# Performance work log

Measured on AMD Instinct MI355X. Metric: run time of the kernel, lower is better.

The kernel has to match this reference:

```python
import jax, jax.numpy as jnp
import numpy as np

VOCAB = 50000
EMB = 200        # embedding_size
CAP = 3          # capitalization_size
IN = EMB + CAP   # LSTM input size = 203
HID = 128        # LSTMCell(128)
B = 256
T = 500          # comment_length
NC = 6           # num_classes
DENSE = 64


def _lstm_scan(x_tbi, W, b):
    """x_tbi: [T,B,IN]. W: [IN+HID, 4*HID] (tf gate order i, j, f, o), b: [4*HID].
    Returns h sequence [T,B,HID]. forget_bias=1.0 as in tf.contrib.rnn.LSTMCell."""
    h0 = jnp.zeros((x_tbi.shape[1], HID), x_tbi.dtype)

    def step(carry, x):
        h, c = carry
        gates = jnp.concatenate([x, h], axis=-1) @ W + b   # [B, 4*HID]
        i, j, f, o = jnp.split(gates, 4, axis=-1)
        c = jax.nn.sigmoid(f + 1.0) * c + jax.nn.sigmoid(i) * jnp.tanh(j)
        h = jax.nn.sigmoid(o) * jnp.tanh(c)
        return (h, c), h

    _, hs = jax.lax.scan(step, (h0, h0), x_tbi)
    return hs


def setup_inputs() -> dict:
    key = jax.random.key(0)
    ks = jax.random.split(key, 12)
    words = jax.random.randint(ks[0], (B, T), 0, VOCAB, dtype=jnp.int32)
    capitals = jax.random.randint(ks[1], (B, T), 0, CAP, dtype=jnp.int32)
    # word embeddings: random trainable table with a trailing zero-padding row
    word_emb = jax.random.normal(ks[2], (VOCAB + 1, EMB), dtype=jnp.float32) * 0.1
    # capitalization embedding: one_hot_embedding_matrix(3) = [eye(3); zeros(1,3)]
    cap_emb = jnp.concatenate([jnp.eye(CAP, dtype=jnp.float32),
                               jnp.zeros((1, CAP), dtype=jnp.float32)], axis=0)
    def glorot(k, shape):
        lim = np.sqrt(6.0 / (shape[0] + shape[1]))
        return jax.random.uniform(k, shape, jnp.float32, -lim, lim)
    W_fw = glorot(ks[3], (IN + HID, 4 * HID))
    b_fw = jnp.zeros((4 * HID,), jnp.float32)
    W_bw = glorot(ks[4], (IN + HID, 4 * HID))
    b_bw = jnp.zeros((4 * HID,), jnp.float32)
    W1 = glorot(ks[5], (2 * HID, DENSE))
    b1 = jnp.zeros((DENSE,), jnp.float32)
    W2 = glorot(ks[6], (DENSE, NC))
    b2 = jnp.zeros((NC,), jnp.float32)
    return {"words": words, "capitals": capitals, "word_emb": word_emb,
            "cap_emb": cap_emb, "W_fw": W_fw, "b_fw": b_fw,
            "W_bw": W_bw, "b_bw": b_bw, "W1": W1, "b1": b1,
            "W2": W2, "b2": b2}


def reference(words, capitals, word_emb, cap_emb, W_fw, b_fw, W_bw, b_bw,
              W1, b1, W2, b2):
    # embedding lookups and concat -> [B, T, 203]
    x = jnp.concatenate([word_emb[words], cap_emb[capitals]], axis=-1)
    x_tbi = jnp.transpose(x, (1, 0, 2))                    # [T, B, IN]
    # forward direction: take output at last timestep
    h_fw_last = _lstm_scan(x_tbi, W_fw, b_fw)[-1]          # [B, HID]
    # backward direction: bidirectional_dynamic_rnn reverses bw outputs back,
    # so outputs[1][:, 0, :] == last state of scan over the reversed sequence
    h_bw_first = _lstm_scan(x_tbi[::-1], W_bw, b_bw)[-1]   # [B, HID]
    rnn_output = jnp.concatenate([h_fw_last, h_bw_first], axis=1)  # [B, 256]
    dense1 = jax.nn.elu(rnn_output @ W1 + b1)              # [B, 64]
    y_hat = jax.nn.sigmoid(dense1 @ W2 + b2)               # [B, NC]
    return y_hat
```

## Files before the change

kernel.cpp:

```cpp
#include <hip/hip_runtime.h>

#define T 500
#define NB 256
#define VROWS 50001
#define EMB 200
#define KPAD 224
#define MPAD 50048
#define LOG2E 1.44269504f

typedef unsigned short u16;
typedef __attribute__((ext_vector_type(8))) __bf16 bf16x8;
typedef __attribute__((ext_vector_type(8))) short short8;
typedef __attribute__((ext_vector_type(4))) float f32x4;
typedef __attribute__((ext_vector_type(4))) u16 u16x4;
typedef __attribute__((ext_vector_type(4))) int i32x4;

__device__ __forceinline__ u16 f2bf(float x) {
  __bf16 h = (__bf16)x;
  return __builtin_bit_cast(u16, h);
}
__device__ __forceinline__ float bf2f(u16 b) {
  union { unsigned u; float f; } v; v.u = ((unsigned)b) << 16;
  return v.f;
}
__device__ __forceinline__ float rcp_(float x) { return __builtin_amdgcn_rcpf(x); }
__device__ __forceinline__ float ex2_(float x) { return __builtin_amdgcn_exp2f(x); }
__device__ __forceinline__ float gsc(int g) { return (g == 1) ? 2.f * LOG2E : -LOG2E; }

__global__ void prep_kernel(const int* __restrict__ words, const int* __restrict__ caps,
                            const float* __restrict__ word_emb,
                            const float* __restrict__ cap_emb,
                            const float* __restrict__ Wfw, const float* __restrict__ bfw,
                            const float* __restrict__ Wbw, const float* __restrict__ bbw,
                            int* __restrict__ wordsT, int* __restrict__ capsT,
                            float* __restrict__ Cproj, u16* __restrict__ Apad,
                            u16* __restrict__ Bt) {
  const int S0 = NB * T;
  const int S1 = MPAD * (KPAD / 4);
  const int S2 = 2 * 512 * KPAD;
  const int S3 = 2 * 4 * 512;
  int tid = blockIdx.x * blockDim.x + threadIdx.x;
  int nthr = gridDim.x * blockDim.x;
  for (int i = tid; i < S0 + S1 + S2 + S3; i += nthr) {
    if (i < S0) {
      int b = i / T, t = i - b * T;
      wordsT[t * NB + b] = words[i];
      capsT[t * NB + b]  = caps[i];
    } else if (i < S0 + S1) {
      int idx = i - S0;
      int v = idx / (KPAD / 4), q = idx - v * (KPAD / 4);
      int k = q * 4;
      u16x4 o;
      if (v < VROWS && k < EMB) {
        const float* p = word_emb + (size_t)v * EMB + k;
        o[0] = f2bf(p[0]); o[1] = f2bf(p[1]); o[2] = f2bf(p[2]); o[3] = f2bf(p[3]);
      } else {
        o[0] = o[1] = o[2] = o[3] = 0;
      }
      *(u16x4*)(Apad + (size_t)v * KPAD + k) = o;
    } else if (i < S0 + S1 + S2) {
      int idx = i - S0 - S1;
      int d = idx / (512 * KPAD), rem = idx - d * (512 * KPAD);
      int colp = rem / KPAD, k = rem - colp * KPAD;
      const float* W = d ? Wbw : Wfw;
      int g = colp & 3, jj = colp >> 2;
      Bt[idx] = (k < EMB) ? f2bf(W[k * 512 + g * 128 + jj] * gsc(g)) : (u16)0;
    } else {
      int idx = i - S0 - S1 - S2;
      int dir = idx >> 11; int c = (idx >> 9) & 3; int colp = idx & 511;
      int j = colp >> 2, g = colp & 3;
      const float* W = dir ? Wbw : Wfw;
      const float* bias = dir ? bbw : bfw;
      float v = bias[g * 128 + j] + (g == 2 ? 1.f : 0.f);
      #pragma unroll
      for (int cc = 0; cc < 3; ++cc)
        v += cap_emb[c * 3 + cc] * W[(200 + cc) * 512 + g * 128 + j];
      Cproj[idx] = v * gsc(g);
    }
  }
}

__global__ __launch_bounds__(256) void vproj_kernel(
    const u16* __restrict__ Apad, const u16* __restrict__ Bt,
    u16* __restrict__ Vfw, u16* __restrict__ Vbw) {
  const int mt = blockIdx.x, nt = blockIdx.y, dir = blockIdx.z;
  const u16* __restrict__ B = Bt + (size_t)dir * 512 * KPAD;
  u16* __restrict__ V = dir ? Vbw : Vfw;

  __shared__ u16 Al[2][128 * 32];
  __shared__ u16 Bl[2][128 * 32];

  const int tid = threadIdx.x;
  const int w = tid >> 6, l = tid & 63;
  const int la = l & 15, lb = l >> 4;
  const int m0 = mt * 128, n0 = nt * 128;

  auto stage = [&](int buf, int ks) {
    int k0 = ks * 32;
    #pragma unroll
    for (int h = 0; h < 2; ++h) {
      int c = w * 128 + h * 64 + l;
      int row = c >> 2, kq = c & 3;
      const u16* ga = Apad + (size_t)(m0 + row) * KPAD + k0 + kq * 8;
      __builtin_amdgcn_global_load_lds(
          (const __attribute__((address_space(1))) void*)ga,
          (__attribute__((address_space(3))) void*)&Al[buf][(w * 128 + h * 64) * 8],
          16, 0, 0);
      const u16* gb = B + (size_t)(n0 + row) * KPAD + k0 + kq * 8;
      __builtin_amdgcn_global_load_lds(
          (const __attribute__((address_space(1))) void*)gb,
          (__attribute__((address_space(3))) void*)&Bl[buf][(w * 128 + h * 64) * 8],
          16, 0, 0);
    }
  };

  f32x4 z = {0.f, 0.f, 0.f, 0.f};
  f32x4 acc[4][4] = {{z,z,z,z},{z,z,z,z},{z,z,z,z},{z,z,z,z}};
  const int wr = w >> 1, wc = w & 1;

  stage(0, 0);
  __syncthreads();
  #pragma unroll 1
  for (int ks = 0; ks < 7; ++ks) {
    int cur = ks & 1;
    if (ks < 6) stage(cur ^ 1, ks + 1);
    bf16x8 af[4], bfr[4];
    #pragma unroll
    for (int m = 0; m < 4; ++m)
      af[m] = *(const bf16x8*)&Al[cur][(wr * 64 + m * 16 + la) * 32 + lb * 8];
    #pragma unroll
    for (int n = 0; n < 4; ++n)
      bfr[n] = *(const bf16x8*)&Bl[cur][(wc * 64 + n * 16 + la) * 32 + lb * 8];
    #pragma unroll
    for (int m = 0; m < 4; ++m)
      #pragma unroll
      for (int n = 0; n < 4; ++n)
        acc[m][n] = __builtin_amdgcn_mfma_f32_16x16x32_bf16(af[m], bfr[n], acc[m][n], 0, 0, 0);
    __syncthreads();
  }

  #pragma unroll
  for (int m = 0; m < 4; ++m) {
    #pragma unroll
    for (int n = 0; n < 4; ++n) {
      #pragma unroll
      for (int r = 0; r < 4; ++r) {
        int v = m0 + wr * 64 + m * 16 + lb * 4 + r;
        int colp = n0 + wc * 64 + n * 16 + la;
        V[(size_t)v * 512 + colp] = f2bf(acc[m][n][r]);
      }
    }
  }
}

template <int PAR>
__device__ __forceinline__ void lstm_step(
    int t, int dir, int b0, int la, int lb, int j,
    const int* __restrict__ wordsT, const int* __restrict__ capsT,
    const u16* __restrict__ V, const float* __restrict__ Cp,
    const bf16x8 (&bfrag)[4][4], u16* __restrict__ hbuf,
    u16x4 (&vw_c)[4], f32x4 (&cp_c)[4],
    i32x4& wi_c, i32x4& ci_c,
    i32x4& wi_g, i32x4& ci_g,
    u16x4 (&vw_g)[4], f32x4 (&cp_g)[4],
    f32x4& cst, f32x4& hl) {
  {
    int ts = t + 4; if (ts > T - 1) ts = T - 1;
    int tt = dir ? (T - 1 - ts) : ts;
    wi_c = *(const i32x4*)(wordsT + tt * NB + b0 + lb * 4);
    ci_c = *(const i32x4*)(capsT + tt * NB + b0 + lb * 4);
  }
  #pragma unroll
  for (int r = 0; r < 4; ++r) {
    vw_g[r] = *(const u16x4*)(V + (size_t)wi_g[r] * 512 + j * 4);
    cp_g[r] = *(const f32x4*)(Cp + ci_g[r] * 512 + j * 4);
  }

  const u16* hb = hbuf + PAR * 2048;
  const int swz = (la & 7) << 3;
  bf16x8 afr[4];
  #pragma unroll
  for (int kk = 0; kk < 4; ++kk)
    afr[kk] = *(const bf16x8*)(hb + ((la * 128 + kk * 32 + lb * 8) ^ swz));

  f32x4 acc0, acc1, acc2, acc3;
  #pragma unroll
  for (int r = 0; r < 4; ++r) {
    acc0[r] = bf2f(vw_c[r][0]) + cp_c[r][0];
    acc1[r] = bf2f(vw_c[r][1]) + cp_c[r][1];
    acc2[r] = bf2f(vw_c[r][2]) + cp_c[r][2];
    acc3[r] = bf2f(vw_c[r][3]) + cp_c[r][3];
  }
  #pragma unroll
  for (int kk = 0; kk < 4; ++kk) {
    acc0 = __builtin_amdgcn_mfma_f32_16x16x32_bf16(afr[kk], bfrag[0][kk], acc0, 0, 0, 0);
    acc1 = __builtin_amdgcn_mfma_f32_16x16x32_bf16(afr[kk], bfrag[1][kk], acc1, 0, 0, 0);
    acc2 = __builtin_amdgcn_mfma_f32_16x16x32_bf16(afr[kk], bfrag[2][kk], acc2, 0, 0, 0);
    acc3 = __builtin_amdgcn_mfma_f32_16x16x32_bf16(afr[kk], bfrag[3][kk], acc3, 0, 0, 0);
  }
  u16* ho = hbuf + (PAR ^ 1) * 2048;
  #pragma unroll
  for (int r = 0; r < 4; ++r) {
    float ig = rcp_(1.f + ex2_(acc0[r]));
    float tj = 1.f - 2.f * rcp_(1.f + ex2_(acc1[r]));
    float fg = rcp_(1.f + ex2_(acc2[r]));
    float cn = fg * cst[r] + ig * tj;
    cst[r] = cn;
    float og = rcp_(1.f + ex2_(acc3[r]));
    float hn = og * (1.f - 2.f * rcp_(1.f + ex2_(2.f * LOG2E * cn)));
    hl[r] = hn;
    int row = lb * 4 + r;
    ho[(row * 128 + j) ^ ((row & 7) << 3)] = f2bf(hn);
  }
  __builtin_amdgcn_sched_barrier(0);
  asm volatile("s_waitcnt lgkmcnt(0)");
  __builtin_amdgcn_s_barrier();
  __builtin_amdgcn_sched_barrier(0);
}

__global__ __launch_bounds__(512, 1) void lstm_kernel(
    const int* __restrict__ wordsT, const int* __restrict__ capsT,
    const u16* __restrict__ Vfw, const u16* __restrict__ Vbw,
    const float* __restrict__ CprojAll, const float* __restrict__ Wfw,
    const float* __restrict__ Wbw, float* __restrict__ rnn) {
  const int dir = blockIdx.x & 1;
  const int chunk = blockIdx.x >> 1;
  const int b0 = chunk * 16;
  const u16* __restrict__ V = dir ? Vbw : Vfw;
  const float* __restrict__ Cp = CprojAll + dir * 4 * 512;
  const float* __restrict__ W = dir ? Wbw : Wfw;

  const int tid = threadIdx.x;
  const int w = tid >> 6, l = tid & 63, la = l & 15, lb = l >> 4;
  const int j = w * 16 + la;

  bf16x8 bfrag[4][4];
  #pragma unroll
  for (int g = 0; g < 4; ++g) {
    #pragma unroll
    for (int kk = 0; kk < 4; ++kk) {
      short8 t8;
      #pragma unroll
      for (int r = 0; r < 8; ++r) {
        int k = kk * 32 + lb * 8 + r;
        t8[r] = (short)f2bf(W[(203 + k) * 512 + g * 128 + j] * gsc(g));
      }
      bfrag[g][kk] = __builtin_bit_cast(bf16x8, t8);
    }
  }

  __shared__ u16 hbuf[2 * 16 * 128];
  for (int i = tid; i < 2 * 16 * 128; i += 512) hbuf[i] = 0;

  f32x4 cst = {0.f, 0.f, 0.f, 0.f};
  f32x4 hl  = {0.f, 0.f, 0.f, 0.f};

  i32x4 wiA, ciA, wiB, ciB, wiC, ciC, wiD, ciD;
  u16x4 vwA[4], vwB[4], vwC[4], vwD[4];
  f32x4 cpA[4], cpB[4], cpC[4], cpD[4];
  {
    int t0 = dir ? (T - 1) : 0;
    int t1 = dir ? (T - 2) : 1;
    int t2 = dir ? (T - 3) : 2;
    int t3 = dir ? (T - 4) : 3;
    wiA = *(const i32x4*)(wordsT + t0 * NB + b0 + lb * 4);
    ciA = *(const i32x4*)(capsT + t0 * NB + b0 + lb * 4);
    wiB = *(const i32x4*)(wordsT + t1 * NB + b0 + lb * 4);
    ciB = *(const i32x4*)(capsT + t1 * NB + b0 + lb * 4);
    wiC = *(const i32x4*)(wordsT + t2 * NB + b0 + lb * 4);
    ciC = *(const i32x4*)(capsT + t2 * NB + b0 + lb * 4);
    wiD = *(const i32x4*)(wordsT + t3 * NB + b0 + lb * 4);
    ciD = *(const i32x4*)(capsT + t3 * NB + b0 + lb * 4);
  }
  #pragma unroll
  for (int r = 0; r < 4; ++r) {
    vwA[r] = *(const u16x4*)(V + (size_t)wiA[r] * 512 + j * 4);
    cpA[r] = *(const f32x4*)(Cp + ciA[r] * 512 + j * 4);
    vwB[r] = *(const u16x4*)(V + (size_t)wiB[r] * 512 + j * 4);
    cpB[r] = *(const f32x4*)(Cp + ciB[r] * 512 + j * 4);
  }
  __syncthreads();

  #pragma unroll 1
  for (int tq = 0; tq < T / 4; ++tq) {
    int t0 = 4 * tq;
    lstm_step<0>(t0,     dir, b0, la, lb, j, wordsT, capsT, V, Cp, bfrag, hbuf,
                 vwA, cpA, wiA, ciA, wiC, ciC, vwC, cpC, cst, hl);
    lstm_step<1>(t0 + 1, dir, b0, la, lb, j, wordsT, capsT, V, Cp, bfrag, hbuf,
                 vwB, cpB, wiB, ciB, wiD, ciD, vwD, cpD, cst, hl);
    lstm_step<0>(t0 + 2, dir, b0, la, lb, j, wordsT, capsT, V, Cp, bfrag, hbuf,
                 vwC, cpC, wiC, ciC, wiA, ciA, vwA, cpA, cst, hl);
    lstm_step<1>(t0 + 3, dir, b0, la, lb, j, wordsT, capsT, V, Cp, bfrag, hbuf,
                 vwD, cpD, wiD, ciD, wiB, ciB, vwB, cpB, cst, hl);
  }

  #pragma unroll
  for (int r = 0; r < 4; ++r)
    rnn[(size_t)(b0 + lb * 4 + r) * 256 + dir * 128 + j] = hl[r];
}

__global__ void head_kernel(const float* __restrict__ rnn, const float* __restrict__ W1,
                            const float* __restrict__ b1, const float* __restrict__ W2,
                            const float* __restrict__ b2, float* __restrict__ out) {
  int b = blockIdx.x;
  int jj = threadIdx.x;
  __shared__ float d1[64];
  float acc = b1[jj];
  const float* r = rnn + b * 256;
  #pragma unroll 4
  for (int k = 0; k < 256; ++k) acc += r[k] * W1[k * 64 + jj];
  d1[jj] = acc > 0.f ? acc : (__expf(acc) - 1.f);
  __syncthreads();
  if (jj < 6) {
    float a2 = b2[jj];
    #pragma unroll 8
    for (int k = 0; k < 64; ++k) a2 += d1[k] * W2[k * 6 + jj];
    out[b * 6 + jj] = rcp_(1.f + __expf(-a2));
  }
}

extern "C" void kernel_launch(void* const* d_in, const int* in_sizes, int n_in,
                              void* d_out, int out_size, void* d_ws, size_t ws_size,
                              hipStream_t stream) {
  (void)in_sizes; (void)n_in; (void)out_size; (void)ws_size;
  const int*   words    = (const int*)  d_in[0];
  const int*   caps     = (const int*)  d_in[1];
  const float* word_emb = (const float*)d_in[2];
  const float* cap_emb  = (const float*)d_in[3];
  const float* Wfw      = (const float*)d_in[4];
  const float* bfw      = (const float*)d_in[5];
  const float* Wbw      = (const float*)d_in[6];
  const float* bbw      = (const float*)d_in[7];
  const float* W1       = (const float*)d_in[8];
  const float* b1       = (const float*)d_in[9];
  const float* W2       = (const float*)d_in[10];
  const float* b2       = (const float*)d_in[11];
  float* out = (float*)d_out;

  char* base = (char*)d_ws;
  size_t off = 0;
  auto alloc = [&](size_t bytes) {
    char* q = base + off;
    off = (off + bytes + 255) & ~(size_t)255;
    return q;
  };
  u16*   Vfw    = (u16*)  alloc((size_t)MPAD * 512 * 2);
  u16*   Vbw    = (u16*)  alloc((size_t)MPAD * 512 * 2);
  u16*   Apad   = (u16*)  alloc((size_t)MPAD * KPAD * 2);
  u16*   Bt     = (u16*)  alloc((size_t)2 * 512 * KPAD * 2);
  int*   wordsT = (int*)  alloc((size_t)T * NB * 4);
  int*   capsT  = (int*)  alloc((size_t)T * NB * 4);
  float* Cproj  = (float*)alloc((size_t)2 * 4 * 512 * 4);
  float* rnn    = (float*)alloc((size_t)256 * 256 * 4);

  hipLaunchKernelGGL(prep_kernel, dim3(2048), dim3(256), 0, stream,
                     words, caps, word_emb, cap_emb, Wfw, bfw, Wbw, bbw,
                     wordsT, capsT, Cproj, Apad, Bt);
  hipLaunchKernelGGL(vproj_kernel, dim3(MPAD / 128, 4, 2), dim3(256), 0, stream,
                     Apad, Bt, Vfw, Vbw);
  hipLaunchKernelGGL(lstm_kernel, dim3(32), dim3(512), 0, stream,
                     wordsT, capsT, Vfw, Vbw, Cproj, Wfw, Wbw, rnn);
  hipLaunchKernelGGL(head_kernel, dim3(256), dim3(64), 0, stream,
                     rnn, W1, b1, W2, b2, out);
}
```

Baseline: 580.0 us.

## Transpose LSTM MFMA operands so each lane owns one batch row

Swaps the MFMA A/B operands so the output tile is laid out as hidden-unit by batch. Each lane then handles a single batch row and four consecutive hidden units. The per-step gather of precomputed input projections becomes one index load per lane plus contiguous 16-byte vector loads, replacing four scattered 8-byte loads. The hidden-state write becomes a single vectorized LDS store, and the rnn output becomes one float4 store. The gate math is rewritten to use fewer reciprocals by combining sigmoid and tanh denominators algebraically, and the MFMA block is bracketed by s_setprio. The combined rational forms may lose accuracy or overflow for large gate inputs.

```diff
diff --git a/kernel.cpp b/kernel.cpp
--- a/kernel.cpp
+++ b/kernel.cpp
@@ -11,9 +11,12 @@
 typedef unsigned short u16;
 typedef __attribute__((ext_vector_type(8))) __bf16 bf16x8;
 typedef __attribute__((ext_vector_type(8))) short short8;
+typedef __attribute__((ext_vector_type(8))) u16 u16x8;
 typedef __attribute__((ext_vector_type(4))) float f32x4;
 typedef __attribute__((ext_vector_type(4))) u16 u16x4;
-typedef __attribute__((ext_vector_type(4))) int i32x4;
+
+#define AS1 __attribute__((address_space(1)))
+#define AS3 __attribute__((address_space(3)))
 
 __device__ __forceinline__ u16 f2bf(float x) {
   __bf16 h = (__bf16)x;
@@ -103,14 +106,12 @@
       int row = c >> 2, kq = c & 3;
       const u16* ga = Apad + (size_t)(m0 + row) * KPAD + k0 + kq * 8;
       __builtin_amdgcn_global_load_lds(
-          (const __attribute__((address_space(1))) void*)ga,
-          (__attribute__((address_space(3))) void*)&Al[buf][(w * 128 + h * 64) * 8],
-          16, 0, 0);
+          (const AS1 void*)ga,
+          (AS3 void*)&Al[buf][(w * 128 + h * 64) * 8], 16, 0, 0);
       const u16* gb = B + (size_t)(n0 + row) * KPAD + k0 + kq * 8;
       __builtin_amdgcn_global_load_lds(
-          (const __attribute__((address_space(1))) void*)gb,
-          (__attribute__((address_space(3))) void*)&Bl[buf][(w * 128 + h * 64) * 8],
-          16, 0, 0);
+          (const AS1 void*)gb,
+          (AS3 void*)&Bl[buf][(w * 128 + h * 64) * 8], 16, 0, 0);
     }
   };
 
@@ -155,63 +156,78 @@
 
 template <int PAR>
 __device__ __forceinline__ void lstm_step(
-    int t, int dir, int b0, int la, int lb, int j,
+    int t, int dir, int b0, int la, int lb, int w, int colbase,
     const int* __restrict__ wordsT, const int* __restrict__ capsT,
     const u16* __restrict__ V, const float* __restrict__ Cp,
     const bf16x8 (&bfrag)[4][4], u16* __restrict__ hbuf,
-    u16x4 (&vw_c)[4], f32x4 (&cp_c)[4],
-    i32x4& wi_c, i32x4& ci_c,
-    i32x4& wi_g, i32x4& ci_g,
-    u16x4 (&vw_g)[4], f32x4 (&cp_g)[4],
+    u16x8 (&vw_c)[2], f32x4 (&cp_c)[4],
+    int& wi_c, int& ci_c,
+    int& wi_g, int& ci_g,
+    u16x8 (&vw_g)[2], f32x4 (&cp_g)[4],
     f32x4& cst, f32x4& hl) {
+  const u16* hb = hbuf + PAR * 2048;
+  const int swz = (la & 7) << 3;
+  bf16x8 afr[4];
+  #pragma unroll
+  for (int kk = 0; kk < 4; ++kk)
+    afr[kk] = *(const bf16x8*)(hb + ((la * 128 + kk * 32 + lb * 8) ^ swz));
+
   {
     int ts = t + 4; if (ts > T - 1) ts = T - 1;
     int tt = dir ? (T - 1 - ts) : ts;
-    wi_c = *(const i32x4*)(wordsT + tt * NB + b0 + lb * 4);
-    ci_c = *(const i32x4*)(capsT + tt * NB + b0 + lb * 4);
-  }
+    wi_c = wordsT[tt * NB + b0 + la];
+    ci_c = capsT[tt * NB + b0 + la];
+  }
+  {
+    const u16* vp = V + (size_t)wi_g * 512 + colbase;
+    vw_g[0] = *(const u16x8*)vp;
+    vw_g[1] = *(const u16x8*)(vp + 8);
+    const float* cp = Cp + ci_g * 512 + colbase;
+    cp_g[0] = *(const f32x4*)(cp + 0);
+    cp_g[1] = *(const f32x4*)(cp + 4);
+    cp_g[2] = *(const f32x4*)(cp + 8);
+    cp_g[3] = *(const f32x4*)(cp + 12);
+  }
+
+  f32x4 acc0, acc1, acc2, acc3;
   #pragma unroll
   for (int r = 0; r < 4; ++r) {
-    vw_g[r] = *(const u16x4*)(V + (size_t)wi_g[r] * 512 + j * 4);
-    cp_g[r] = *(const f32x4*)(Cp + ci_g[r] * 512 + j * 4);
-  }
-
-  const u16* hb = hbuf + PAR * 2048;
-  const int swz = (la & 7) << 3;
-  bf16x8 afr[4];
-  #pragma unroll
-  for (int kk = 0; kk < 4; ++kk)
-    afr[kk] = *(const bf16x8*)(hb + ((la * 128 + kk * 32 + lb * 8) ^ swz));
-
-  f32x4 acc0, acc1, acc2, acc3;
+    const u16x8& xh = vw_c[r >> 1];
+    int base = (r & 1) * 4;
+    acc0[r] = bf2f(xh[base + 0]) + cp_c[r][0];
+    acc1[r] = bf2f(xh[base + 1]) + cp_c[r][1];
+    acc2[r] = bf2f(xh[base + 2]) + cp_c[r][2];
+    acc3[r] = bf2f(xh[base + 3]) + cp_c[r][3];
+  }
+  __builtin_amdgcn_s_setprio(1);
+  #pragma unroll
+  for (int kk = 0; kk < 4; ++kk) {
+    acc0 = __builtin_amdgcn_mfma_f32_16x16x32_bf16(bfrag[0][kk], afr[kk], acc0, 0, 0, 0);
+    acc1 = __builtin_amdgcn_mfma_f32_16x16x32_bf16(bfrag[1][kk], afr[kk], acc1, 0, 0, 0);
+    acc2 = __builtin_amdgcn_mfma_f32_16x16x32_bf16(bfrag[2][kk], afr[kk], acc2, 0, 0, 0);
+    acc3 = __builtin_amdgcn_mfma_f32_16x16x32_bf16(bfrag[3][kk], afr[kk], acc3, 0, 0, 0);
+  }
+  __builtin_amdgcn_s_setprio(0);
+  u16* ho = hbuf + (PAR ^ 1) * 2048;
+  u16x4 hw;
   #pragma unroll
   for (int r = 0; r < 4; ++r) {
-    acc0[r] = bf2f(vw_c[r][0]) + cp_c[r][0];
-    acc1[r] = bf2f(vw_c[r][1]) + cp_c[r][1];
-    acc2[r] = bf2f(vw_c[r][2]) + cp_c[r][2];
-    acc3[r] = bf2f(vw_c[r][3]) + cp_c[r][3];
-  }
-  #pragma unroll
-  for (int kk = 0; kk < 4; ++kk) {
-    acc0 = __builtin_amdgcn_mfma_f32_16x16x32_bf16(afr[kk], bfrag[0][kk], acc0, 0, 0, 0);
-    acc1 = __builtin_amdgcn_mfma_f32_16x16x32_bf16(afr[kk], bfrag[1][kk], acc1, 0, 0, 0);
-    acc2 = __builtin_amdgcn_mfma_f32_16x16x32_bf16(afr[kk], bfrag[2][kk], acc2, 0, 0, 0);
-    acc3 = __builtin_amdgcn_mfma_f32_16x16x32_bf16(afr[kk], bfrag[3][kk], acc3, 0, 0, 0);
-  }
-  u16* ho = hbuf + (PAR ^ 1) * 2048;
-  #pragma unroll
-  for (int r = 0; r < 4; ++r) {
-    float ig = rcp_(1.f + ex2_(acc0[r]));
-    float tj = 1.f - 2.f * rcp_(1.f + ex2_(acc1[r]));
-    float fg = rcp_(1.f + ex2_(acc2[r]));
-    float cn = fg * cst[r] + ig * tj;
+    float ei = ex2_(acc0[r]);
+    float ej = ex2_(acc1[r]);
+    float ef = ex2_(acc2[r]);
+    float eo = ex2_(acc3[r]);
+    float pij = (1.f + ei) * (1.f + ej);
+    float pf  = 1.f + ef;
+    float num = cst[r] * pij + (ej - 1.f) * pf;
+    float cn  = num * rcp_(pij * pf);
     cst[r] = cn;
-    float og = rcp_(1.f + ex2_(acc3[r]));
-    float hn = og * (1.f - 2.f * rcp_(1.f + ex2_(2.f * LOG2E * cn)));
+    float E = ex2_(2.f * LOG2E * cn);
+    float hn = (E - 1.f) * rcp_((1.f + eo) * (1.f + E));
     hl[r] = hn;
-    int row = lb * 4 + r;
-    ho[(row * 128 + j) ^ ((row & 7) << 3)] = f2bf(hn);
-  }
+    hw[r] = f2bf(hn);
+  }
+  *(u16x4*)&hbuf[((PAR ^ 1) * 2048) + ((la * 128 + w * 16 + lb * 4) ^ swz)] = hw;
+  (void)ho;
   __builtin_amdgcn_sched_barrier(0);
   asm volatile("s_waitcnt lgkmcnt(0)");
   __builtin_amdgcn_s_barrier();
@@ -233,6 +249,7 @@
   const int tid = threadIdx.x;
   const int w = tid >> 6, l = tid & 63, la = l & 15, lb = l >> 4;
   const int j = w * 16 + la;
+  const int colbase = w * 64 + lb * 16;
 
   bf16x8 bfrag[4][4];
   #pragma unroll
@@ -255,48 +272,47 @@
   f32x4 cst = {0.f, 0.f, 0.f, 0.f};
   f32x4 hl  = {0.f, 0.f, 0.f, 0.f};
 
-  i32x4 wiA, ciA, wiB, ciB, wiC, ciC, wiD, ciD;
-  u16x4 vwA[4], vwB[4], vwC[4], vwD[4];
+  int wiA, ciA, wiB, ciB, wiC, ciC, wiD, ciD;
+  u16x8 vwA[2], vwB[2], vwC[2], vwD[2];
   f32x4 cpA[4], cpB[4], cpC[4], cpD[4];
   {
     int t0 = dir ? (T - 1) : 0;
     int t1 = dir ? (T - 2) : 1;
     int t2 = dir ? (T - 3) : 2;
     int t3 = dir ? (T - 4) : 3;
-    wiA = *(const i32x4*)(wordsT + t0 * NB + b0 + lb * 4);
-    ciA = *(const i32x4*)(capsT + t0 * NB + b0 + lb * 4);
-    wiB = *(const i32x4*)(wordsT + t1 * NB + b0 + lb * 4);
-    ciB = *(const i32x4*)(capsT + t1 * NB + b0 + lb * 4);
-    wiC = *(const i32x4*)(wordsT + t2 * NB + b0 + lb * 4);
-    ciC = *(const i32x4*)(capsT + t2 * NB + b0 + lb * 4);
-    wiD = *(const i32x4*)(wordsT + t3 * NB + b0 + lb * 4);
-    ciD = *(const i32x4*)(capsT + t3 * NB + b0 + lb * 4);
-  }
-  #pragma unroll
-  for (int r = 0; r < 4; ++r) {
-    vwA[r] = *(const u16x4*)(V + (size_t)wiA[r] * 512 + j * 4);
-    cpA[r] = *(const f32x4*)(Cp + ciA[r] * 512 + j * 4);
-    vwB[r] = *(const u16x4*)(V + (size_t)wiB[r] * 512 + j * 4);
-    cpB[r] = *(const f32x4*)(Cp + ciB[r] * 512 + j * 4);
+    wiA = wordsT[t0 * NB + b0 + la]; ciA = capsT[t0 * NB + b0 + la];
+    wiB = wordsT[t1 * NB + b0 + la]; ciB = capsT[t1 * NB + b0 + la];
+    wiC = wordsT[t2 * NB + b0 + la]; ciC = capsT[t2 * NB + b0 + la];
+    wiD = wordsT[t3 * NB + b0 + la]; ciD = capsT[t3 * NB + b0 + la];
+  }
+  {
+    const u16* vp0 = V + (size_t)wiA * 512 + colbase;
+    vwA[0] = *(const u16x8*)vp0; vwA[1] = *(const u16x8*)(vp0 + 8);
+    const float* cp0 = Cp + ciA * 512 + colbase;
+    cpA[0] = *(const f32x4*)(cp0 + 0); cpA[1] = *(const f32x4*)(cp0 + 4);
+    cpA[2] = *(const f32x4*)(cp0 + 8); cpA[3] = *(const f32x4*)(cp0 + 12);
+    const u16* vp1 = V + (size_t)wiB * 512 + colbase;
+    vwB[0] = *(const u16x8*)vp1; vwB[1] = *(const u16x8*)(vp1 + 8);
+    const float* cp1 = Cp + ciB * 512 + colbase;
+    cpB[0] = *(const f32x4*)(cp1 + 0); cpB[1] = *(const f32x4*)(cp1 + 4);
+    cpB[2] = *(const f32x4*)(cp1 + 8); cpB[3] = *(const f32x4*)(cp1 + 12);
   }
   __syncthreads();
 
   #pragma unroll 1
   for (int tq = 0; tq < T / 4; ++tq) {
     int t0 = 4 * tq;
-    lstm_step<0>(t0,     dir, b0, la, lb, j, wordsT, capsT, V, Cp, bfrag, hbuf,
-                 vwA, cpA, wiA, ciA, wiC, ciC, vwC, cpC, cst, hl);
-    lstm_step<1>(t0 + 1, dir, b0, la, lb, j, wordsT, capsT, V, Cp, bfrag, hbuf,
-                 vwB, cpB, wiB, ciB, wiD, ciD, vwD, cpD, cst, hl);
-    lstm_step<0>(t0 + 2, dir, b0, la, lb, j, wordsT, capsT, V, Cp, bfrag, hbuf,
-                 vwC, cpC, wiC, ciC, wiA, ciA, vwA, cpA, cst, hl);
-    lstm_step<1>(t0 + 3, dir, b0, la, lb, j, wordsT, capsT, V, Cp, bfrag, hbuf,
-                 vwD, cpD, wiD, ciD, wiB, ciB, vwB, cpB, cst, hl);
-  }
-
-  #pragma unroll
-  for (int r = 0; r < 4; ++r)
-    rnn[(size_t)(b0 + lb * 4 + r) * 256 + dir * 128 + j] = hl[r];
+    lstm_step<0>(t0,     dir, b0, la, lb, w, colbase, wordsT, capsT, V, Cp,
+                 bfrag, hbuf, vwA, cpA, wiA, ciA, wiC, ciC, vwC, cpC, cst, hl);
+    lstm_step<1>(t0 + 1, dir, b0, la, lb, w, colbase, wordsT, capsT, V, Cp,
+                 bfrag, hbuf, vwB, cpB, wiB, ciB, wiD, ciD, vwD, cpD, cst, hl);
+    lstm_step<0>(t0 + 2, dir, b0, la, lb, w, colbase, wordsT, capsT, V, Cp,
+                 bfrag, hbuf, vwC, cpC, wiC, ciC, wiA, ciA, vwA, cpA, cst, hl);
+    lstm_step<1>(t0 + 3, dir, b0, la, lb, w, colbase, wordsT, capsT, V, Cp,
+                 bfrag, hbuf, vwD, cpD, wiD, ciD, wiB, ciB, vwB, cpB, cst, hl);
+  }
+
+  *(f32x4*)&rnn[(size_t)(b0 + la) * 256 + dir * 128 + w * 16 + lb * 4] = hl;
 }
 
 __global__ void head_kernel(const float* __restrict__ rnn, const float* __restrict__ W1,
```

Result: slower. 681.8 us (+17.6%).
